# Optimization experiments

Hardware: AMD Instinct MI355X
Metric: run time of the kernel (lower is better)

The kernel has to match this reference:

```python
import jax, jax.numpy as jnp
import numpy as np

TEMP = 0.05
ALPHA = 0.1
EPS = 1e-12


def setup_inputs() -> dict:
    key = jax.random.key(0)
    k1, k2, k3, k4 = jax.random.split(key, 4)
    bs, emb_dim, n_class, n_aux = 16384, 512, 2000, 5
    features = jax.random.normal(k1, (bs, emb_dim), dtype=jnp.float32)
    word_embed = jax.random.normal(k2, (n_class, emb_dim), dtype=jnp.float32)
    label = jax.random.randint(k3, (bs,), 0, n_class)
    aux = jax.random.randint(k4, (bs, n_aux), 0, n_class)
    return {"features": features, "word_embed": word_embed, "label": label, "aux": aux}


def _cosine_logits(features, word_embed):
    # F.normalize(x, dim=-1): x / max(||x||, eps)
    f = features / jnp.maximum(jnp.linalg.norm(features, axis=-1, keepdims=True), EPS)
    w = word_embed / jnp.maximum(jnp.linalg.norm(word_embed, axis=-1, keepdims=True), EPS)
    return jnp.matmul(f, w.T) / TEMP  # (bs, n_class)


def reference(features, word_embed, label, aux):
    pred = _cosine_logits(features, word_embed)
    lse = jax.nn.logsumexp(pred, axis=1)                                  # log sum exp per row
    tgt = jnp.take_along_axis(pred, label[:, None], axis=1)[:, 0]         # pred[i, target[i]]
    # normal cross entropy: mean_i(-pred[i,t_i] + log sum exp(pred[i]))
    loss_normal = jnp.mean(-tgt + lse)
    # label-smoothing CE: -(1-a)*pred[i,t_i] + lse - (a/n_aux)*sum_j pred[i, aux[i,j]]
    single_alpha = ALPHA / aux.shape[-1]
    aux_logits = jnp.take_along_axis(pred, aux, axis=1)                   # (bs, n_aux)
    loss_ls = jnp.mean(-(1.0 - ALPHA) * tgt + lse - single_alpha * jnp.sum(aux_logits, axis=1))
    loss = 0.5 * (loss_normal + loss_ls)
    acc = jnp.mean((jnp.argmax(pred, axis=1) == label).astype(jnp.float32))
    return loss, acc
```

## Files before the change

### kernel.cpp

```cpp
#include <hip/hip_runtime.h>
#include <hip/hip_bf16.h>
#include <hip/hip_fp8.h>
#include <stdint.h>

#define BS   16384
#define NC   2000
#define NCP  2048
#define EMB  512
#define NAUX 5
#define NCHUNK 32
#define GBLK 4096

typedef __bf16 bf16x8 __attribute__((ext_vector_type(8)));
typedef float  f32x4  __attribute__((ext_vector_type(4)));

__global__ __launch_bounds__(256) void norm_kernel(
    const float* __restrict__ feat, const float* __restrict__ wemb,
    unsigned char* __restrict__ fn8, unsigned char* __restrict__ wn8,
    __bf16* __restrict__ fnb, __bf16* __restrict__ wnb)
{
    const int sub = threadIdx.x & 15;
    const int row = blockIdx.x * 16 + (threadIdx.x >> 4);

    if (row >= BS + NC) {
        const int pr = row - BS;
        uint4 z4 = {0, 0, 0, 0};
        ((uint4*)(wn8 + (size_t)pr * EMB))[sub * 2]     = z4;
        ((uint4*)(wn8 + (size_t)pr * EMB))[sub * 2 + 1] = z4;
        bf16x8 z = {};
        bf16x8* d = (bf16x8*)(wnb + (size_t)pr * EMB) + sub * 4;
        #pragma unroll
        for (int i = 0; i < 4; ++i) d[i] = z;
        return;
    }
    const float* src;
    unsigned char* dst8;
    __bf16* dstb;
    if (row < BS) { src = feat + (size_t)row * EMB;
                    dst8 = fn8 + (size_t)row * EMB;        dstb = fnb + (size_t)row * EMB; }
    else          { src = wemb + (size_t)(row - BS) * EMB;
                    dst8 = wn8 + (size_t)(row - BS) * EMB; dstb = wnb + (size_t)(row - BS) * EMB; }

    const float4* s4 = (const float4*)src + sub * 8;
    float4 x[8];
    float ss = 0.f;
    #pragma unroll
    for (int i = 0; i < 8; ++i) {
        x[i] = s4[i];
        ss += x[i].x * x[i].x + x[i].y * x[i].y + x[i].z * x[i].z + x[i].w * x[i].w;
    }
    #pragma unroll
    for (int m = 1; m < 16; m <<= 1) ss += __shfl_xor(ss, m, 64);
    const float scale = 1.0f / fmaxf(sqrtf(ss), 1e-12f);

    float v[32];
    #pragma unroll
    for (int i = 0; i < 8; ++i) {
        v[4*i]   = x[i].x * scale; v[4*i+1] = x[i].y * scale;
        v[4*i+2] = x[i].z * scale; v[4*i+3] = x[i].w * scale;
    }
    bf16x8* db = (bf16x8*)dstb + sub * 4;
    #pragma unroll
    for (int i = 0; i < 4; ++i) {
        bf16x8 o;
        #pragma unroll
        for (int jj = 0; jj < 8; ++jj) o[jj] = (__bf16)v[8*i + jj];
        db[i] = o;
    }
    unsigned char pb[32];
    #pragma unroll
    for (int i = 0; i < 32; ++i)
        pb[i] = __hip_cvt_float_to_fp8(v[i], __HIP_SATFINITE, __HIP_E4M3);
    uint4* d8 = (uint4*)(dst8 + sub * 32);
    d8[0] = *(const uint4*)(pb);
    d8[1] = *(const uint4*)(pb + 16);
}

__global__ __launch_bounds__(256) void main_kernel(
    const unsigned char* __restrict__ fn8, const unsigned char* __restrict__ wn8,
    float* __restrict__ es_p, unsigned* __restrict__ key_p)
{
    __shared__ __align__(16) unsigned char As[128 * 256];
    __shared__ __align__(16) unsigned char Bs[128 * 256];

    const int tid   = threadIdx.x;
    const int lane  = tid & 63;
    const int l15   = lane & 15;
    const int quad  = lane >> 4;
    const int wv    = tid >> 6;
    const int wvM   = wv >> 1;
    const int wvN   = wv & 1;
    const int xcd   = blockIdx.x & 7;
    const int j     = blockIdx.x >> 3;
    const int mTile = xcd * 16 + (j >> 4);
    const int nTile = j & 15;

    const unsigned char* fbase = fn8 + (size_t)mTile * 128 * EMB;
    const unsigned char* wbase = wn8 + (size_t)nTile * 128 * EMB;

    const int rIn = lane >> 4;
    const int cPh = lane & 15;
    f32x4 acc[4][4] = {};

    #pragma unroll
    for (int kk = 0; kk < 2; ++kk) {
        __syncthreads();
        #pragma unroll
        for (int p = 0; p < 8; ++p) {
            const int slot = wv * 8 + p;
            const int row  = slot * 4 + rIn;
            const int cLog = cPh ^ (row & 7);
            const size_t goff = (size_t)row * EMB + kk * 256 + cLog * 16;
            __builtin_amdgcn_global_load_lds(
                (const __attribute__((address_space(1))) void*)(fbase + goff),
                (__attribute__((address_space(3))) void*)(As + slot * 1024), 16, 0, 0);
            __builtin_amdgcn_global_load_lds(
                (const __attribute__((address_space(1))) void*)(wbase + goff),
                (__attribute__((address_space(3))) void*)(Bs + slot * 1024), 16, 0, 0);
        }
        __builtin_amdgcn_s_waitcnt(0);
        __syncthreads();

        #pragma unroll
        for (int kc = 0; kc < 8; ++kc) {
            long aF[4], bF[4];
            const int c16  = kc * 2 + (quad >> 1);
            const int hoff = (quad & 1) << 3;
            #pragma unroll
            for (int i = 0; i < 4; ++i) {
                const int ar = wvM * 64 + i * 16 + l15;
                const int br = wvN * 64 + i * 16 + l15;
                const int ca = ((c16 ^ (l15 & 7)) << 4) + hoff;
                aF[i] = *(const long*)(As + ar * 256 + ca);
                bF[i] = *(const long*)(Bs + br * 256 + ca);
            }
            #pragma unroll
            for (int mi = 0; mi < 4; ++mi)
                #pragma unroll
                for (int ni = 0; ni < 4; ++ni)
                    acc[mi][ni] = __builtin_amdgcn_mfma_f32_16x16x32_fp8_fp8(
                        aF[mi], bF[ni], acc[mi][ni], 0, 0, 0);
        }
    }

    const float C20 = 28.853900817779268f;
    const int chunk = nTile * 2 + wvN;
    #pragma unroll
    for (int mi = 0; mi < 4; ++mi) {
        float    es[4] = {0.f, 0.f, 0.f, 0.f};
        unsigned km[4] = {0u, 0u, 0u, 0u};
        #pragma unroll
        for (int ni = 0; ni < 4; ++ni) {
            const int col = nTile * 128 + wvN * 64 + ni * 16 + l15;
            const unsigned colenc = 2047u - (unsigned)col;
            const bool valid = (col < NC);
            #pragma unroll
            for (int r = 0; r < 4; ++r) {
                float v = valid ? acc[mi][ni][r] : -3.0f;
                es[r] += exp2f((v - 1.0f) * C20);
                unsigned u = __float_as_uint(v);
                unsigned k = u ^ (unsigned)(((int)u >> 31) | 0x80000000);
                unsigned pk = (k & 0xFFFFF800u) | colenc;
                km[r] = pk > km[r] ? pk : km[r];
            }
        }
        #pragma unroll
        for (int r = 0; r < 4; ++r) {
            #pragma unroll
            for (int m = 1; m < 16; m <<= 1) {
                es[r] += __shfl_xor(es[r], m, 64);
                unsigned x = __shfl_xor(km[r], m, 64);
                km[r] = x > km[r] ? x : km[r];
            }
        }
        if (l15 == 0) {
            #pragma unroll
            for (int r = 0; r < 4; ++r) {
                const int row = mTile * 128 + wvM * 64 + mi * 16 + quad * 4 + r;
                es_p [(size_t)row * NCHUNK + chunk] = es[r];
                key_p[(size_t)row * NCHUNK + chunk] = km[r];
            }
        }
    }
}

__global__ __launch_bounds__(256) void gather_fin_kernel(
    const __bf16* __restrict__ fnb, const __bf16* __restrict__ wnb,
    const int* __restrict__ label, const int* __restrict__ aux,
    const float* __restrict__ es_p, const unsigned* __restrict__ key_p,
    float* __restrict__ blkpart)
{
    const int lane = threadIdx.x & 63;
    const int wv   = threadIdx.x >> 6;
    const int row  = blockIdx.x * 4 + wv;

    bf16x8 f8 = *((const bf16x8*)fnb + (size_t)row * (EMB / 8) + lane);
    float fv[8];
    #pragma unroll
    for (int j = 0; j < 8; ++j) fv[j] = (float)f8[j];

    const int lab = label[row];
    int cols[6];
    cols[0] = lab;
    #pragma unroll
    for (int j = 0; j < NAUX; ++j) cols[j + 1] = aux[row * NAUX + j];

    float res[6];
    #pragma unroll
    for (int c = 0; c < 6; ++c) {
        bf16x8 w8 = *((const bf16x8*)wnb + (size_t)cols[c] * (EMB / 8) + lane);
        float d = 0.f;
        #pragma unroll
        for (int j = 0; j < 8; ++j) d += fv[j] * (float)w8[j];
        #pragma unroll
        for (int m = 1; m < 64; m <<= 1) d += __shfl_xor(d, m, 64);
        res[c] = d;
    }
    const float tgt  = res[0] * 20.0f;
    const float auxs = (res[1] + res[2] + res[3] + res[4] + res[5]) * 20.0f;

    const int c = lane & 31;
    float    es = es_p [(size_t)row * NCHUNK + c];
    unsigned k  = key_p[(size_t)row * NCHUNK + c];
    #pragma unroll
    for (int m = 1; m < 32; m <<= 1) {
        es += __shfl_xor(es, m, 64);
        unsigned x = __shfl_xor(k, m, 64);
        k = x > k ? x : k;
    }
    const int amax = 2047 - (int)(k & 0x7FFu);
    const float loss = 20.0f + logf(es) - 0.95f * tgt - 0.01f * auxs;
    const float acc  = (amax == lab) ? 1.0f : 0.0f;

    __shared__ float sl[4], sa[4];
    if (lane == 0) { sl[wv] = loss; sa[wv] = acc; }
    __syncthreads();
    if (threadIdx.x == 0) {
        blkpart[blockIdx.x]        = sl[0] + sl[1] + sl[2] + sl[3];
        blkpart[GBLK + blockIdx.x] = sa[0] + sa[1] + sa[2] + sa[3];
    }
}

__global__ __launch_bounds__(256) void fin2_kernel(
    const float* __restrict__ blkpart, float* __restrict__ out)
{
    float l = 0.f, a = 0.f;
    for (int i = threadIdx.x; i < GBLK; i += 256) {
        l += blkpart[i];
        a += blkpart[GBLK + i];
    }
    #pragma unroll
    for (int m = 1; m < 64; m <<= 1) {
        l += __shfl_xor(l, m, 64);
        a += __shfl_xor(a, m, 64);
    }
    __shared__ float sl[4], sa[4];
    const int wv = threadIdx.x >> 6;
    if ((threadIdx.x & 63) == 0) { sl[wv] = l; sa[wv] = a; }
    __syncthreads();
    if (threadIdx.x == 0) {
        out[0] = (sl[0] + sl[1] + sl[2] + sl[3]) / (float)BS;
        out[1] = (sa[0] + sa[1] + sa[2] + sa[3]) / (float)BS;
    }
}

extern "C" void kernel_launch(void* const* d_in, const int* in_sizes, int n_in,
                              void* d_out, int out_size, void* d_ws, size_t ws_size,
                              hipStream_t stream)
{
    const float* feat  = (const float*)d_in[0];
    const float* wemb  = (const float*)d_in[1];
    const int*   label = (const int*)d_in[2];
    const int*   aux   = (const int*)d_in[3];

    char* ws = (char*)d_ws;
    unsigned char* fn8     = (unsigned char*)(ws);
    unsigned char* wn8     = (unsigned char*)(ws + 8388608);
    __bf16*        fnb     = (__bf16*)(ws + 9437184);
    __bf16*        wnb     = (__bf16*)(ws + 26214400);
    float*         es_p    = (float*)(ws + 28311552);
    unsigned*      key_p   = (unsigned*)(ws + 30408704);
    float*         blkpart = (float*)(ws + 32505856);
    float*         out     = (float*)d_out;

    hipLaunchKernelGGL(norm_kernel, dim3((BS + NCP) / 16), dim3(256), 0, stream,
                       feat, wemb, fn8, wn8, fnb, wnb);
    hipLaunchKernelGGL(main_kernel, dim3((BS / 128) * (NCP / 128)), dim3(256), 0, stream,
                       fn8, wn8, es_p, key_p);
    hipLaunchKernelGGL(gather_fin_kernel, dim3(GBLK), dim3(256), 0, stream,
                       fnb, wnb, label, aux, es_p, key_p, blkpart);
    hipLaunchKernelGGL(fin2_kernel, dim3(1), dim3(256), 0, stream, blkpart, out);
}
```

Baseline: 147.6 us.

## Double-buffer fp8 GEMM K-loop in LDS to overlap global loads with MFMA

The K loop is split into four 128-byte stages held in two ping-pong LDS buffers. The next stage is issued with global_load_lds while MFMAs run on the current buffer, where before the kernel loaded and then computed in two serial halves. Total LDS per block stays the same. Each K step now needs a barrier, and the extra synchronisation plus the smaller per-step work could offset the overlap gain.

```diff
diff --git a/kernel.cpp b/kernel.cpp
--- a/kernel.cpp
+++ b/kernel.cpp
@@ -80,8 +80,8 @@
     const unsigned char* __restrict__ fn8, const unsigned char* __restrict__ wn8,
     float* __restrict__ es_p, unsigned* __restrict__ key_p)
 {
-    __shared__ __align__(16) unsigned char As[128 * 256];
-    __shared__ __align__(16) unsigned char Bs[128 * 256];
+    __shared__ __align__(16) unsigned char As[2][128 * 128];
+    __shared__ __align__(16) unsigned char Bs[2][128 * 128];
 
     const int tid   = threadIdx.x;
     const int lane  = tid & 63;
@@ -98,31 +98,38 @@
     const unsigned char* fbase = fn8 + (size_t)mTile * 128 * EMB;
     const unsigned char* wbase = wn8 + (size_t)nTile * 128 * EMB;
 
-    const int rIn = lane >> 4;
-    const int cPh = lane & 15;
+    const int rIn8 = lane >> 3;
+    const int cLog = (lane & 7) ^ rIn8;
+
     f32x4 acc[4][4] = {};
 
-    #pragma unroll
-    for (int kk = 0; kk < 2; ++kk) {
-        __syncthreads();
-        #pragma unroll
-        for (int p = 0; p < 8; ++p) {
-            const int slot = wv * 8 + p;
-            const int row  = slot * 4 + rIn;
-            const int cLog = cPh ^ (row & 7);
-            const size_t goff = (size_t)row * EMB + kk * 256 + cLog * 16;
+    auto STAGE = [&](int t, int buf) {
+        #pragma unroll
+        for (int p = 0; p < 4; ++p) {
+            const int slot = wv * 4 + p;
+            const int row  = slot * 8 + rIn8;
+            const size_t goff = (size_t)row * EMB + (size_t)t * 128 + (size_t)cLog * 16;
             __builtin_amdgcn_global_load_lds(
                 (const __attribute__((address_space(1))) void*)(fbase + goff),
-                (__attribute__((address_space(3))) void*)(As + slot * 1024), 16, 0, 0);
+                (__attribute__((address_space(3))) void*)(&As[buf][slot * 1024]), 16, 0, 0);
             __builtin_amdgcn_global_load_lds(
                 (const __attribute__((address_space(1))) void*)(wbase + goff),
-                (__attribute__((address_space(3))) void*)(Bs + slot * 1024), 16, 0, 0);
-        }
-        __builtin_amdgcn_s_waitcnt(0);
-        __syncthreads();
-
-        #pragma unroll
-        for (int kc = 0; kc < 8; ++kc) {
+                (__attribute__((address_space(3))) void*)(&Bs[buf][slot * 1024]), 16, 0, 0);
+        }
+    };
+
+    STAGE(0, 0);
+    asm volatile("s_waitcnt vmcnt(0)" ::: "memory");
+    __builtin_amdgcn_s_barrier();
+    asm volatile("" ::: "memory");
+
+    #pragma unroll
+    for (int t = 0; t < 4; ++t) {
+        const int cur = t & 1;
+        if (t < 3) STAGE(t + 1, cur ^ 1);
+
+        #pragma unroll
+        for (int kc = 0; kc < 4; ++kc) {
             long aF[4], bF[4];
             const int c16  = kc * 2 + (quad >> 1);
             const int hoff = (quad & 1) << 3;
@@ -131,8 +138,8 @@
                 const int ar = wvM * 64 + i * 16 + l15;
                 const int br = wvN * 64 + i * 16 + l15;
                 const int ca = ((c16 ^ (l15 & 7)) << 4) + hoff;
-                aF[i] = *(const long*)(As + ar * 256 + ca);
-                bF[i] = *(const long*)(Bs + br * 256 + ca);
+                aF[i] = *(const long*)(&As[cur][ar * 128 + ca]);
+                bF[i] = *(const long*)(&Bs[cur][br * 128 + ca]);
             }
             #pragma unroll
             for (int mi = 0; mi < 4; ++mi)
@@ -140,6 +147,12 @@
                 for (int ni = 0; ni < 4; ++ni)
                     acc[mi][ni] = __builtin_amdgcn_mfma_f32_16x16x32_fp8_fp8(
                         aF[mi], bF[ni], acc[mi][ni], 0, 0, 0);
+        }
+
+        if (t < 3) {
+            asm volatile("s_waitcnt vmcnt(0) lgkmcnt(0)" ::: "memory");
+            __builtin_amdgcn_s_barrier();
+            asm volatile("" ::: "memory");
         }
     }
 
```

After: 150.9 us. 1.02x slower.
